# Optimization experiments

Hardware: AMD Instinct MI355X
Metric: run time of the kernel (lower is better)

Reference implementation:

```python
import jax, jax.numpy as jnp
import numpy as np

PAD = -100

def _make_offsets(key, batch, src_len, n_words, valid_len):
    ofs = jnp.sort(jax.random.randint(key, (batch, src_len), 0, n_words), axis=1)
    # ensure max valid offset is n_words-1 so target_length == max+1
    ofs = ofs.at[:, valid_len - 1].set(n_words - 1)
    pos = jnp.arange(src_len)[None, :]
    return jnp.where(pos < valid_len, ofs, PAD).astype(jnp.int64)

def setup_inputs() -> dict:
    key = jax.random.key(0)
    k1, k2 = jax.random.split(key)
    batch, src_len, dim = 8, 4096, 1024
    n_words = 2048
    valid_len = src_len - 256  # trailing PAD region
    hidden_states = jax.random.normal(k1, (batch, src_len, dim), dtype=jnp.float32)
    word_offsets = _make_offsets(k2, batch, src_len, n_words, valid_len)
    return {"hidden_states": hidden_states, "word_offsets": word_offsets,
            "target_length": n_words}

def reference(hidden_states, word_offsets, target_length):
    # Faithful to WordPooler with take=_take_first: for each word, gather the
    # FIRST subword token (stop at first -100), then scatter-mean per word
    # (include_self=False -> untouched words stay zero).
    B, S, D = hidden_states.shape
    T = target_length
    # 'break' semantics: everything after the first PAD is invalid
    valid = jnp.cumprod((word_offsets != PAD).astype(jnp.int32), axis=1).astype(bool)
    prev = jnp.concatenate(
        [jnp.full((B, 1), -1, dtype=word_offsets.dtype), word_offsets[:, :-1]], axis=1)
    first = valid & (word_offsets != prev)  # [B, S] first-token-of-word mask
    # route non-selected tokens to a dump bucket (index T per batch)
    tgt = jnp.where(first, word_offsets, T)
    flat_tgt = (jnp.arange(B)[:, None] * (T + 1) + tgt).reshape(-1)  # [B*S]
    flat_h = hidden_states.reshape(B * S, D)
    w = first.reshape(-1).astype(hidden_states.dtype)  # selection weights
    sums = jnp.zeros((B * (T + 1), D), dtype=hidden_states.dtype)
    sums = sums.at[flat_tgt].add(flat_h * w[:, None])
    counts = jnp.zeros((B * (T + 1),), dtype=hidden_states.dtype).at[flat_tgt].add(w)
    out = sums / jnp.maximum(counts, 1.0)[:, None]  # zero-count words stay 0
    return out.reshape(B, T + 1, D)[:, :T, :]
```

## Files before the change

### kernel.cpp

```cpp
#include <hip/hip_runtime.h>


typedef float v4f __attribute__((ext_vector_type(4)));

__global__ void __launch_bounds__(256)
wp_scatter_kernel(const int* __restrict__ ofs, int* __restrict__ src,
                  int S, int T) {
    const int s = blockIdx.x * 256 + threadIdx.x;
    const int b = blockIdx.y;
    if (s >= S) return;
    const int* __restrict__ row = ofs + (size_t)b * S;
    const int v = row[s];
    if (v < 0) return;
    const int prev = (s == 0) ? -1 : row[s - 1];
    if (v != prev) src[(size_t)b * T + v] = s;
}

__global__ void __launch_bounds__(256)
wp_gather_kernel(const float* __restrict__ hs, const int* __restrict__ ofs,
                 const int* __restrict__ src, float* __restrict__ out,
                 int S, int T, int D) {
    const int wave = threadIdx.x >> 6;
    const int lane = threadIdx.x & 63;
    const int t = blockIdx.x * 4 + wave;
    const int b = blockIdx.y;
    const size_t word = (size_t)b * T + t;
    const int s = src[word];

    bool present = false;
    if ((unsigned)s < (unsigned)S) {
        const int* __restrict__ row = ofs + (size_t)b * S;
        const int v = row[s];
        const int prev = (s == 0) ? -1 : row[s - 1];
        present = (v == t) & (prev != t);
    }

    v4f* __restrict__ o = (v4f*)(out + word * (size_t)D);
    if (present) {
        const v4f* __restrict__ in =
            (const v4f*)(hs + ((size_t)b * S + s) * (size_t)D);
        v4f r0 = in[lane];
        v4f r1 = in[lane + 64];
        v4f r2 = in[lane + 128];
        v4f r3 = in[lane + 192];
        o[lane]       = r0;
        o[lane + 64]  = r1;
        o[lane + 128] = r2;
        o[lane + 192] = r3;
    } else {
        const v4f z = (v4f)(0.f);
        o[lane]       = z;
        o[lane + 64]  = z;
        o[lane + 128] = z;
        o[lane + 192] = z;
    }
}

extern "C" void kernel_launch(void* const* d_in, const int* in_sizes, int n_in,
                              void* d_out, int out_size, void* d_ws, size_t ws_size,
                              hipStream_t stream) {
    const float* hs  = (const float*)d_in[0];
    const int*   ofs = (const int*)d_in[1];
    float* out = (float*)d_out;
    int* src = (int*)d_ws;

    const int B = 8;
    const int BS = in_sizes[1];
    const int S = BS / B;
    const int D = in_sizes[0] / BS;
    const int T = out_size / (B * D);

    dim3 g1((S + 255) / 256, B);
    wp_scatter_kernel<<<g1, 256, 0, stream>>>(ofs, src, S, T);

    dim3 g2(T / 4, B);
    wp_gather_kernel<<<g2, 256, 0, stream>>>(hs, ofs, src, out, S, T, D);
}
```

Before: 28.63 us.

## Fuse index scatter and gather into single token-driven copy kernel

Replaces the two-kernel scheme (scatter first-token index into workspace, then per-word gather) with one kernel where each wave handles a token position. A first-of-word token copies its hidden row to the output and zero-fills any skipped word rows since the previous offset; the first PAD token zero-fills any trailing words. This removes a kernel launch and the workspace round-trip, at the cost of launching many waves that exit immediately and uneven per-wave work when gaps are large.

```diff
diff --git a/kernel.cpp b/kernel.cpp
--- a/kernel.cpp
+++ b/kernel.cpp
@@ -4,55 +4,44 @@
 typedef float v4f __attribute__((ext_vector_type(4)));
 
 __global__ void __launch_bounds__(256)
-wp_scatter_kernel(const int* __restrict__ ofs, int* __restrict__ src,
-                  int S, int T) {
-    const int s = blockIdx.x * 256 + threadIdx.x;
-    const int b = blockIdx.y;
-    if (s >= S) return;
-    const int* __restrict__ row = ofs + (size_t)b * S;
-    const int v = row[s];
-    if (v < 0) return;
-    const int prev = (s == 0) ? -1 : row[s - 1];
-    if (v != prev) src[(size_t)b * T + v] = s;
-}
-
-__global__ void __launch_bounds__(256)
-wp_gather_kernel(const float* __restrict__ hs, const int* __restrict__ ofs,
-                 const int* __restrict__ src, float* __restrict__ out,
-                 int S, int T, int D) {
+wp_scatter_copy(const float* __restrict__ hs, const int* __restrict__ ofs,
+                float* __restrict__ out, int S, int T, int D) {
     const int wave = threadIdx.x >> 6;
     const int lane = threadIdx.x & 63;
-    const int t = blockIdx.x * 4 + wave;
+    const int s = blockIdx.x * 4 + wave;
     const int b = blockIdx.y;
-    const size_t word = (size_t)b * T + t;
-    const int s = src[word];
 
-    bool present = false;
-    if ((unsigned)s < (unsigned)S) {
-        const int* __restrict__ row = ofs + (size_t)b * S;
-        const int v = row[s];
-        const int prev = (s == 0) ? -1 : row[s - 1];
-        present = (v == t) & (prev != t);
-    }
+    const int* __restrict__ row = ofs + (size_t)b * S;
+    const int v    = row[s];
+    const int prev = (s == 0) ? -1 : row[s - 1];
 
-    v4f* __restrict__ o = (v4f*)(out + word * (size_t)D);
-    if (present) {
+    const int nv = D >> 2;
+    const v4f z = (v4f)(0.f);
+
+    if (v >= 0) {
+        if (v == prev) return;
         const v4f* __restrict__ in =
             (const v4f*)(hs + ((size_t)b * S + s) * (size_t)D);
         v4f r0 = in[lane];
         v4f r1 = in[lane + 64];
         v4f r2 = in[lane + 128];
         v4f r3 = in[lane + 192];
+        for (int w = prev + 1; w < v; ++w) {
+            v4f* __restrict__ o = (v4f*)(out + ((size_t)b * T + w) * (size_t)D);
+            #pragma unroll 4
+            for (int j = lane; j < nv; j += 64) o[j] = z;
+        }
+        v4f* __restrict__ o = (v4f*)(out + ((size_t)b * T + v) * (size_t)D);
         o[lane]       = r0;
         o[lane + 64]  = r1;
         o[lane + 128] = r2;
         o[lane + 192] = r3;
-    } else {
-        const v4f z = (v4f)(0.f);
-        o[lane]       = z;
-        o[lane + 64]  = z;
-        o[lane + 128] = z;
-        o[lane + 192] = z;
+    } else if (prev >= 0) {
+        for (int w = prev + 1; w < T; ++w) {
+            v4f* __restrict__ o = (v4f*)(out + ((size_t)b * T + w) * (size_t)D);
+            #pragma unroll 4
+            for (int j = lane; j < nv; j += 64) o[j] = z;
+        }
     }
 }
 
@@ -62,7 +51,6 @@
     const float* hs  = (const float*)d_in[0];
     const int*   ofs = (const int*)d_in[1];
     float* out = (float*)d_out;
-    int* src = (int*)d_ws;
 
     const int B = 8;
     const int BS = in_sizes[1];
@@ -70,9 +58,6 @@
     const int D = in_sizes[0] / BS;
     const int T = out_size / (B * D);
 
-    dim3 g1((S + 255) / 256, B);
-    wp_scatter_kernel<<<g1, 256, 0, stream>>>(ofs, src, S, T);
-
-    dim3 g2(T / 4, B);
-    wp_gather_kernel<<<g2, 256, 0, stream>>>(hs, ofs, src, out, S, T, D);
+    dim3 grid(S / 4, B);
+    wp_scatter_copy<<<grid, 256, 0, stream>>>(hs, ofs, out, S, T, D);
 }
```

After: 40.90 us. +42.9%, slower.
